# Kernel optimization log

Measured on AMD Instinct MI355X. Metric: run time of the kernel, lower is better.

Reference implementation:

```python
import jax, jax.numpy as jnp
import numpy as np

BETA = 0.9
THRESHOLD = 1.0
N_IN, N_HID, N_OUT = 784, 2048, 10
BATCH = 128
T_STEPS = 32


def _spike(x):
    # snnTorch heaviside fire: spk = 1 where (mem - threshold) > 0
    return (x > 0).astype(x.dtype)


def setup_inputs() -> dict:
    key = jax.random.key(0)
    ks = jax.random.split(key, 6)

    def lin(k, fan_in, fan_out):
        bound = 1.0 / np.sqrt(fan_in)
        kw, kb = jax.random.split(k)
        W = jax.random.uniform(kw, (fan_out, fan_in), minval=-bound, maxval=bound, dtype=jnp.float32)
        b = jax.random.uniform(kb, (fan_out,), minval=-bound, maxval=bound, dtype=jnp.float32)
        return W, b

    W0, b0 = lin(ks[0], N_IN, N_HID)
    W1, b1 = lin(ks[1], N_HID, N_HID)
    W2, b2 = lin(ks[2], N_HID, N_HID)
    W3, b3 = lin(ks[3], N_HID, N_HID)
    W4, b4 = lin(ks[4], N_HID, N_OUT)
    input_tensor = jax.random.uniform(ks[5], (BATCH, N_IN), dtype=jnp.float32)
    return {"input_tensor": input_tensor,
            "W0": W0, "W1": W1, "W2": W2, "W3": W3, "W4": W4,
            "b0": b0, "b1": b1, "b2": b2, "b3": b3, "b4": b4,
            "time_steps": T_STEPS}


def reference(input_tensor, W0, W1, W2, W3, W4, b0, b1, b2, b3, b4, time_steps):
    Ws = [W0, W1, W2, W3, W4]
    bs = [b0, b1, b2, b3, b4]
    n_lif = len(Ws) + 1  # 6 LIF layers
    batch = input_tensor.shape[0]
    dims = [N_IN, N_HID, N_HID, N_HID, N_HID, N_OUT]  # membrane shapes per LIF
    dtype = input_tensor.dtype

    def step(mems, _):
        cur = input_tensor  # same static input injected every step (as in the torch loop)
        new_mems = []
        var_list = []
        count_list = []
        spk_last = None
        for i in range(n_lif):
            # snnTorch Leaky (reset_mechanism='subtract'):
            # reset computed from PREVIOUS membrane (detached), then decay + input
            reset = jax.lax.stop_gradient((mems[i] > THRESHOLD).astype(dtype))
            mem = BETA * mems[i] + cur - reset * THRESHOLD
            spk = _spike(mem - THRESHOLD)
            new_mems.append(mem)
            count_list.append(spk.sum(axis=1).mean(axis=0))  # sum over features, mean over batch
            if i < n_lif - 1:
                var_list.append(jnp.var(mem, ddof=1))  # torch.var default: unbiased
                cur = spk @ Ws[i].T + bs[i]
            else:
                spk_last = spk
        return tuple(new_mems), (spk_last, jnp.stack(var_list), jnp.stack(count_list))

    mems0 = tuple(jnp.zeros((batch, d), dtype=dtype) for d in dims)
    _, (spike_out, vars_t, counts_t) = jax.lax.scan(step, mems0, None, length=time_steps)

    mean_var_mems = vars_t.mean(axis=0)                       # [n_linears] = [5]
    normalized_spike_counts = counts_t.sum(axis=0) / (time_steps * batch)  # [n_lif] = [6]
    return mean_var_mems, spike_out, normalized_spike_counts
```

## Files before the change

kernel.cpp:

```cpp
#include <hip/hip_runtime.h>
#include <stdint.h>

#define BETA 0.9f
#define NIN 784
#define KA0 832
#define NHID 2048
#define BATCH 128
#define TSTEPS 32
#define MROWS 4096

typedef float f32x4 __attribute__((ext_vector_type(4)));
typedef int   i32x4 __attribute__((ext_vector_type(4)));

#define S1F 0x1p-11f
#define S2F 0x1p-19f
#define S3F 0x1p-27f

__device__ __forceinline__ float nofuse(float x) {
  asm volatile("" : "+v"(x));
  return x;
}

typedef __attribute__((address_space(1))) const unsigned int gas_uint;
typedef __attribute__((address_space(3))) unsigned int las_uint;
__device__ __forceinline__ void gload_lds16(const void* g, void* l) {
  __builtin_amdgcn_global_load_lds((gas_uint*)g, (las_uint*)l, 16, 0, 0);
}

static const size_t SZ_WS0  = (size_t)3 * 2048 * KA0;
static const size_t SZ_WSH  = (size_t)3 * 2048 * 2048;
static const size_t SZ_W4T  = (size_t)2048 * 16 * 4;
static const size_t SZ_SPK  = (size_t)MROWS * 2048;
static const size_t SZ_CUR  = (size_t)MROWS * 2048 * 4;
static const size_t SZ_CUR5 = (size_t)MROWS * 16 * 4;
static const size_t SZ_VST  = (size_t)5 * TSTEPS * 256 * 2 * 4;
static const size_t SZ_CST  = (size_t)6 * TSTEPS * 256 * 4;

static const size_t OFF_WS0  = 0;
static const size_t OFF_WS1  = OFF_WS0 + SZ_WS0;
static const size_t OFF_WS2  = OFF_WS1 + SZ_WSH;
static const size_t OFF_WS3  = OFF_WS2 + SZ_WSH;
static const size_t OFF_W4T  = OFF_WS3 + SZ_WSH;
static const size_t OFF_SPKA = OFF_W4T + SZ_W4T;
static const size_t OFF_SPKB = OFF_SPKA + SZ_SPK;
static const size_t OFF_CUR  = OFF_SPKB + SZ_SPK;
static const size_t OFF_CUR5 = OFF_CUR + SZ_CUR;
static const size_t OFF_VST  = OFF_CUR5 + SZ_CUR5;
static const size_t OFF_CST  = OFF_VST + SZ_VST;

__global__ void k_wsplit(const float* __restrict__ W, signed char* __restrict__ dst,
                         int nrows, int kvalid, int kpad) {
  int idx = blockIdx.x * blockDim.x + threadIdx.x;
  int kq = kvalid >> 2;
  if (idx >= nrows * kq) return;
  int row = idx / kq, k0 = (idx - row * kq) * 4;
  const float* src = W + (size_t)row * kvalid + k0;
  signed char p1[4], p2[4], p3[4];
#pragma unroll
  for (int e = 0; e < 4; ++e) {
    float f = src[e];
    float q1 = rintf(f * 2048.0f);
    float r1 = f - q1 * S1F;
    float q2 = rintf(r1 * 524288.0f);
    q2 = fminf(127.f, fmaxf(-127.f, q2));
    float r2 = r1 - q2 * S2F;
    float q3 = rintf(r2 * 134217728.0f);
    q3 = fminf(127.f, fmaxf(-127.f, q3));
    p1[e] = (signed char)(int)q1;
    p2[e] = (signed char)(int)q2;
    p3[e] = (signed char)(int)q3;
  }
  size_t base = (size_t)row * kpad + k0;
  size_t plane = (size_t)nrows * kpad;
  *(char4*)(dst + base)             = make_char4(p1[0], p1[1], p1[2], p1[3]);
  *(char4*)(dst + plane + base)     = make_char4(p2[0], p2[1], p2[2], p2[3]);
  *(char4*)(dst + 2 * plane + base) = make_char4(p3[0], p3[1], p3[2], p3[3]);
}

__global__ void k_w4t(const float* __restrict__ W4, float* __restrict__ w4t) {
  int k = blockIdx.x * blockDim.x + threadIdx.x;
  if (k >= 2048) return;
#pragma unroll
  for (int c = 0; c < 16; ++c)
    w4t[(size_t)k * 16 + c] = (c < 10) ? W4[(size_t)c * 2048 + k] : 0.f;
}

__global__ __launch_bounds__(256, 2) void k_gemm3p(
    const signed char* __restrict__ A,
    const signed char* __restrict__ B,
    float* __restrict__ C,
    int N, int Ka) {
  __shared__ __align__(16) signed char smem[2][32768];
  const int tid = threadIdx.x;
  const int lane = tid & 63, wv = tid >> 6;

  const int bid = blockIdx.x;
  const int xcd = bid & 7, lid = bid >> 3;
  const int by = (xcd >> 1) * 8 + (lid >> 3);
  const int bx = (xcd & 1) * 8 + (lid & 7);
  const int m0 = by * 128, n0 = bx * 128;
  const int NT = Ka >> 6;

  i32x4 acc0[4][4], acc1[4][4], acc2[4][4];
#pragma unroll
  for (int i = 0; i < 4; ++i)
#pragma unroll
    for (int j = 0; j < 4; ++j) {
      acc0[i][j] = (i32x4){0, 0, 0, 0};
      acc1[i][j] = (i32x4){0, 0, 0, 0};
      acc2[i][j] = (i32x4){0, 0, 0, 0};
    }

  auto stage_part = [&](int buf, int kt, int i0, int i1) {
    const int koff = kt * 64;
    const signed char* Abase = A + (size_t)m0 * Ka + koff;
    for (int i = i0; i < i1; ++i) {
      int c = i * 256 + tid;
      const signed char* src;
      if (c < 512) {
        int row = c >> 2, kb = c & 3;
        int gkb = kb ^ ((row >> 1) & 3);
        src = Abase + (size_t)row * Ka + gkb * 16;
      } else {
        int cb = c - 512;
        int s = cb >> 9, cc = cb & 511;
        int row = cc >> 2, kb = cc & 3;
        int gkb = kb ^ ((row >> 1) & 3);
        src = B + ((size_t)s * N + n0 + row) * Ka + koff + gkb * 16;
      }
      gload_lds16(src, &smem[buf][(i * 256 + wv * 64) * 16]);
    }
  };

  const int wm = wv >> 1, wn = wv & 1;
  const int g = lane >> 4, rr = lane & 15;

  auto readA = [&](int p, i32x4* a) {
#pragma unroll
    for (int mf = 0; mf < 4; ++mf) {
      int row = wm * 64 + mf * 16 + rr;
      int slot = g ^ ((row >> 1) & 3);
      a[mf] = *(const i32x4*)&smem[p][row * 64 + slot * 16];
    }
  };
  auto readB = [&](int p, int s, i32x4* b) {
#pragma unroll
    for (int nf = 0; nf < 4; ++nf) {
      int row = wn * 64 + nf * 16 + rr;
      int slot = g ^ ((row >> 1) & 3);
      b[nf] = *(const i32x4*)&smem[p][8192 + s * 8192 + row * 64 + slot * 16];
    }
  };
  auto cluster = [&](i32x4* a, i32x4* b, i32x4 (*acc)[4]) {
    __builtin_amdgcn_s_setprio(1);
#pragma unroll
    for (int mf = 0; mf < 4; ++mf)
#pragma unroll
      for (int nf = 0; nf < 4; ++nf)
        acc[mf][nf] = __builtin_amdgcn_mfma_i32_16x16x64_i8(a[mf], b[nf], acc[mf][nf], 0, 0, 0);
    __builtin_amdgcn_s_setprio(0);
  };

#define PHASE_SYNC(nimm)                                   \
  asm volatile("s_waitcnt vmcnt(" #nimm ")" ::: "memory"); \
  __builtin_amdgcn_sched_barrier(0);                       \
  __builtin_amdgcn_s_barrier();                            \
  __builtin_amdgcn_sched_barrier(0);

  stage_part(0, 0, 0, 8);

  for (int kt = 0; kt < NT - 1; ++kt) {
    const int p = kt & 1;
    i32x4 a[4], b[4];
    PHASE_SYNC(4)
    stage_part(p ^ 1, kt + 1, 0, 2);
    readA(p, a);
    readB(p, 0, b);
    cluster(a, b, acc0);
    PHASE_SYNC(4)
    stage_part(p ^ 1, kt + 1, 2, 6);
    readB(p, 1, b);
    cluster(a, b, acc1);
    PHASE_SYNC(6)
    stage_part(p ^ 1, kt + 1, 6, 8);
    readB(p, 2, b);
    cluster(a, b, acc2);
  }
  {
    const int p = (NT - 1) & 1;
    i32x4 a[4], b[4];
    PHASE_SYNC(4)
    readA(p, a);
    readB(p, 0, b);
    cluster(a, b, acc0);
    PHASE_SYNC(2)
    readB(p, 1, b);
    cluster(a, b, acc1);
    PHASE_SYNC(0)
    readB(p, 2, b);
    cluster(a, b, acc2);
  }
#undef PHASE_SYNC

#pragma unroll
  for (int mf = 0; mf < 4; ++mf)
#pragma unroll
    for (int nf = 0; nf < 4; ++nf) {
      int col = n0 + wn * 64 + nf * 16 + rr;
#pragma unroll
      for (int v = 0; v < 4; ++v) {
        int row = m0 + wm * 64 + mf * 16 + g * 4 + v;
        float f = S1F * (float)acc0[mf][nf][v];
        f = __fmaf_rn(S2F, (float)acc1[mf][nf][v], f);
        f = __fmaf_rn(S3F, (float)acc2[mf][nf][v], f);
        C[(size_t)row * N + col] = f;
      }
    }
}

__global__ __launch_bounds__(128) void k_scan0(
    const float* __restrict__ input, signed char* __restrict__ spk0,
    float* __restrict__ vstats, int* __restrict__ cstats) {
  const int b = blockIdx.x, tid = threadIdx.x;
  const int j0 = tid * 8;
  const bool act = (j0 < NIN);
  const int lane = tid & 63, wv = tid >> 6;
  __shared__ float ssum[2][TSTEPS], ssq[2][TSTEPS];
  __shared__ int scnt[2][TSTEPS];
  float iv[8];
  if (act) {
    const float* ip = input + (size_t)b * NIN + j0;
    float4 c0 = *(const float4*)ip, c1 = *(const float4*)(ip + 4);
    iv[0]=c0.x; iv[1]=c0.y; iv[2]=c0.z; iv[3]=c0.w;
    iv[4]=c1.x; iv[5]=c1.y; iv[6]=c1.z; iv[7]=c1.w;
  } else {
#pragma unroll
    for (int e = 0; e < 8; ++e) iv[e] = 0.f;
  }
  float mem[8] = {0,0,0,0,0,0,0,0};
  for (int t = 0; t < TSTEPS; ++t) {
    float sum = 0.f, sq = 0.f; int cnt = 0;
    unsigned long long pk = 0;
#pragma unroll
    for (int e = 0; e < 8; ++e) {
      float reset = mem[e] > 1.0f ? 1.0f : 0.0f;
      float t1 = nofuse(BETA * mem[e]);
      float t2 = nofuse(t1 + iv[e]);
      float mn = t2 - reset;
      mem[e] = mn;
      int s = mn > 1.0f;
      pk |= (unsigned long long)(s ? 1u : 0u) << (8 * e);
      sum += mn; sq = __fmaf_rn(mn, mn, sq); cnt += s;
    }
    if (act)
      *(unsigned long long*)(spk0 + (size_t)(t * BATCH + b) * KA0 + j0) = pk;
#pragma unroll
    for (int o = 32; o > 0; o >>= 1) {
      sum += __shfl_down(sum, o, 64);
      sq  += __shfl_down(sq, o, 64);
      cnt += __shfl_down(cnt, o, 64);
    }
    if (lane == 0) { ssum[wv][t] = sum; ssq[wv][t] = sq; scnt[wv][t] = cnt; }
  }
  __syncthreads();
  if (tid < TSTEPS) {
    int t = tid;
    float s = ssum[0][t] + ssum[1][t];
    float q = ssq[0][t] + ssq[1][t];
    int c = scnt[0][t] + scnt[1][t];
    vstats[((size_t)(0 * TSTEPS + t) * 256 + b) * 2 + 0] = s;
    vstats[((size_t)(0 * TSTEPS + t) * 256 + b) * 2 + 1] = q;
    cstats[(0 * TSTEPS + t) * 256 + b] = c;
  }
}

__global__ __launch_bounds__(128) void k_scan(
    const float* __restrict__ cur, const float* __restrict__ bias,
    signed char* __restrict__ spk, float* __restrict__ vstats,
    int* __restrict__ cstats, int layer) {
  const int blk = blockIdx.x;
  const int b = blk >> 1, half = blk & 1;
  const int tid = threadIdx.x;
  const int j0 = half * 1024 + tid * 8;
  const int lane = tid & 63, wv = tid >> 6;
  __shared__ float ssum[2][TSTEPS], ssq[2][TSTEPS];
  __shared__ int scnt[2][TSTEPS];
  float bs[8];
  {
    const float* bp = bias + j0;
    float4 c0 = *(const float4*)bp, c1 = *(const float4*)(bp + 4);
    bs[0]=c0.x; bs[1]=c0.y; bs[2]=c0.z; bs[3]=c0.w;
    bs[4]=c1.x; bs[5]=c1.y; bs[6]=c1.z; bs[7]=c1.w;
  }
  float mem[8] = {0,0,0,0,0,0,0,0};
  for (int t = 0; t < TSTEPS; ++t) {
    size_t off = (size_t)(t * BATCH + b) * 2048 + j0;
    const float* cp = cur + off;
    float4 c0 = *(const float4*)cp, c1 = *(const float4*)(cp + 4);
    float cv[8] = {c0.x, c0.y, c0.z, c0.w, c1.x, c1.y, c1.z, c1.w};
    float sum = 0.f, sq = 0.f; int cnt = 0;
    unsigned long long pk = 0;
#pragma unroll
    for (int e = 0; e < 8; ++e) {
      float cc = nofuse(cv[e] + bs[e]);
      float reset = mem[e] > 1.0f ? 1.0f : 0.0f;
      float t1 = nofuse(BETA * mem[e]);
      float t2 = nofuse(t1 + cc);
      float mn = t2 - reset;
      mem[e] = mn;
      int s = mn > 1.0f;
      pk |= (unsigned long long)(s ? 1u : 0u) << (8 * e);
      sum += mn; sq = __fmaf_rn(mn, mn, sq); cnt += s;
    }
    *(unsigned long long*)(spk + (size_t)(t * BATCH + b) * 2048 + j0) = pk;
#pragma unroll
    for (int o = 32; o > 0; o >>= 1) {
      sum += __shfl_down(sum, o, 64);
      sq  += __shfl_down(sq, o, 64);
      cnt += __shfl_down(cnt, o, 64);
    }
    if (lane == 0) { ssum[wv][t] = sum; ssq[wv][t] = sq; scnt[wv][t] = cnt; }
  }
  __syncthreads();
  if (tid < TSTEPS) {
    int t = tid;
    float s = ssum[0][t] + ssum[1][t];
    float q = ssq[0][t] + ssq[1][t];
    int c = scnt[0][t] + scnt[1][t];
    vstats[((size_t)(layer * TSTEPS + t) * 256 + blk) * 2 + 0] = s;
    vstats[((size_t)(layer * TSTEPS + t) * 256 + blk) * 2 + 1] = q;
    cstats[(layer * TSTEPS + t) * 256 + blk] = c;
  }
}

__global__ __launch_bounds__(256) void k_gemm4(
    const signed char* __restrict__ spk, const float* __restrict__ w4t,
    float* __restrict__ out) {
  int idx = blockIdx.x * 256 + threadIdx.x;
  int r = idx >> 4, c = idx & 15;
  const signed char* sp = spk + (size_t)r * 2048;
  float acc = 0.f;
  for (int k = 0; k < 2048; k += 4) {
    char4 s4 = *(const char4*)(sp + k);
    acc = __fmaf_rn((float)s4.x, w4t[(size_t)(k + 0) * 16 + c], acc);
    acc = __fmaf_rn((float)s4.y, w4t[(size_t)(k + 1) * 16 + c], acc);
    acc = __fmaf_rn((float)s4.z, w4t[(size_t)(k + 2) * 16 + c], acc);
    acc = __fmaf_rn((float)s4.w, w4t[(size_t)(k + 3) * 16 + c], acc);
  }
  out[(size_t)r * 16 + c] = acc;
}

__global__ __launch_bounds__(640) void k_scan5(
    const float* __restrict__ cur5, const float* __restrict__ b4,
    float* __restrict__ spike_out, int* __restrict__ cstats) {
  const int tid = threadIdx.x;
  const int idx = blockIdx.x * 640 + tid;
  const int b = idx / 10, j = idx - b * 10;
  const int lane = tid & 63, wv = tid >> 6;
  __shared__ int scnt[10][TSTEPS];
  const float bias = b4[j];
  float mem = 0.f;
  for (int t = 0; t < TSTEPS; ++t) {
    float cc = nofuse(cur5[(size_t)(t * BATCH + b) * 16 + j] + bias);
    float reset = mem > 1.0f ? 1.0f : 0.0f;
    float t1 = nofuse(BETA * mem);
    float t2 = nofuse(t1 + cc);
    float mn = t2 - reset;
    mem = mn;
    int s = mn > 1.0f;
    spike_out[(size_t)t * 1280 + b * 10 + j] = s ? 1.0f : 0.0f;
    int cnt = s;
#pragma unroll
    for (int o = 32; o > 0; o >>= 1) cnt += __shfl_down(cnt, o, 64);
    if (lane == 0) scnt[wv][t] = cnt;
  }
  __syncthreads();
  if (tid < TSTEPS) {
    int t = tid, c = 0;
#pragma unroll
    for (int w = 0; w < 10; ++w) c += scnt[w][t];
    cstats[(5 * TSTEPS + t) * 256 + blockIdx.x] = c;
  }
}

__global__ __launch_bounds__(512) void k_final(
    const float* __restrict__ vstats, const int* __restrict__ cstats,
    float* __restrict__ d_out) {
  __shared__ float varLDS[5][TSTEPS];
  __shared__ float cntLDS[6][TSTEPS];
  int tid = threadIdx.x;
  if (tid < 160) {
    int l = tid / 32, t = tid - l * 32;
    double s = 0.0, q = 0.0;
    for (int b = 0; b < 256; ++b) {
      s += (double)vstats[((size_t)(l * TSTEPS + t) * 256 + b) * 2 + 0];
      q += (double)vstats[((size_t)(l * TSTEPS + t) * 256 + b) * 2 + 1];
    }
    double n = (l == 0) ? (double)(BATCH * NIN) : (double)(BATCH * NHID);
    varLDS[l][t] = (float)((q - s * s / n) / (n - 1.0));
  } else if (tid < 352) {
    int i = (tid - 160) / 32, t = (tid - 160) - i * 32;
    int c = 0;
    for (int b = 0; b < 256; ++b) c += cstats[(i * TSTEPS + t) * 256 + b];
    cntLDS[i][t] = (float)c * (1.0f / 128.0f);
  }
  __syncthreads();
  if (tid < 5) {
    float a = 0.f;
    for (int t = 0; t < TSTEPS; ++t) a = __fadd_rn(a, varLDS[tid][t]);
    d_out[tid] = a / 32.0f;
  } else if (tid >= 8 && tid < 14) {
    int i = tid - 8;
    float a = 0.f;
    for (int t = 0; t < TSTEPS; ++t) a = __fadd_rn(a, cntLDS[i][t]);
    d_out[40965 + i] = a / 4096.0f;
  }
}

extern "C" void kernel_launch(void* const* d_in, const int* in_sizes, int n_in,
                              void* d_out, int out_size, void* d_ws, size_t ws_size,
                              hipStream_t stream) {
  const float* input = (const float*)d_in[0];
  const float* W0 = (const float*)d_in[1];
  const float* W1 = (const float*)d_in[2];
  const float* W2 = (const float*)d_in[3];
  const float* W3 = (const float*)d_in[4];
  const float* W4 = (const float*)d_in[5];
  const float* b0 = (const float*)d_in[6];
  const float* b1 = (const float*)d_in[7];
  const float* b2 = (const float*)d_in[8];
  const float* b3 = (const float*)d_in[9];
  const float* b4 = (const float*)d_in[10];

  uint8_t* ws = (uint8_t*)d_ws;
  signed char* ws0  = (signed char*)(ws + OFF_WS0);
  signed char* ws1  = (signed char*)(ws + OFF_WS1);
  signed char* ws2  = (signed char*)(ws + OFF_WS2);
  signed char* ws3  = (signed char*)(ws + OFF_WS3);
  float* w4t        = (float*)(ws + OFF_W4T);
  signed char* spkA = (signed char*)(ws + OFF_SPKA);
  signed char* spkB = (signed char*)(ws + OFF_SPKB);
  float* cur        = (float*)(ws + OFF_CUR);
  float* cur5       = (float*)(ws + OFF_CUR5);
  float* vst        = (float*)(ws + OFF_VST);
  int* cst          = (int*)(ws + OFF_CST);
  float* out        = (float*)d_out;

  hipMemsetAsync(ws + OFF_VST, 0, SZ_VST + SZ_CST, stream);
  hipMemsetAsync(ws + OFF_SPKA, 0, (size_t)TSTEPS * BATCH * KA0, stream);
  hipMemsetAsync(ws + OFF_WS0, 0, SZ_WS0, stream);

  {
    int thr = 2048 * (NIN / 4);
    k_wsplit<<<(thr + 255) / 256, 256, 0, stream>>>(W0, ws0, 2048, NIN, KA0);
  }
  {
    int thr = 2048 * (2048 / 4);
    int gb = (thr + 255) / 256;
    k_wsplit<<<gb, 256, 0, stream>>>(W1, ws1, 2048, 2048, 2048);
    k_wsplit<<<gb, 256, 0, stream>>>(W2, ws2, 2048, 2048, 2048);
    k_wsplit<<<gb, 256, 0, stream>>>(W3, ws3, 2048, 2048, 2048);
  }
  k_w4t<<<8, 256, 0, stream>>>(W4, w4t);

  k_scan0<<<BATCH, 128, 0, stream>>>(input, spkA, vst, cst);
  k_gemm3p<<<512, 256, 0, stream>>>(spkA, ws0, cur, 2048, KA0);
  k_scan<<<256, 128, 0, stream>>>(cur, b0, spkB, vst, cst, 1);
  k_gemm3p<<<512, 256, 0, stream>>>(spkB, ws1, cur, 2048, 2048);
  k_scan<<<256, 128, 0, stream>>>(cur, b1, spkA, vst, cst, 2);
  k_gemm3p<<<512, 256, 0, stream>>>(spkA, ws2, cur, 2048, 2048);
  k_scan<<<256, 128, 0, stream>>>(cur, b2, spkB, vst, cst, 3);
  k_gemm3p<<<512, 256, 0, stream>>>(spkB, ws3, cur, 2048, 2048);
  k_scan<<<256, 128, 0, stream>>>(cur, b3, spkA, vst, cst, 4);
  k_gemm4<<<256, 256, 0, stream>>>(spkA, w4t, cur5);
  k_scan5<<<2, 640, 0, stream>>>(cur5, b4, out + 5, cst);
  k_final<<<1, 512, 0, stream>>>(vst, cst, out);
}
```

Before: 402.0 us.

## Merge weight-split launches, simplify GEMM staging to one sync per k-tile, widen final reduction

Combines the four weight quantization-split kernels into a single launch to cut launch overhead. Replaces the GEMM's three-phase partial staging and waitcnt scheme with one full-tile prefetch per iteration behind a single barrier, folding the epilogue iteration into the loop. Doubles the threads in the final statistics reduction and combines thread pairs with a shuffle. The simpler GEMM pipeline may give up some of the load/MFMA interleaving the phased version had.

```diff
diff --git a/kernel.cpp b/kernel.cpp
--- a/kernel.cpp
+++ b/kernel.cpp
@@ -48,9 +48,9 @@
 static const size_t OFF_VST  = OFF_CUR5 + SZ_CUR5;
 static const size_t OFF_CST  = OFF_VST + SZ_VST;
 
-__global__ void k_wsplit(const float* __restrict__ W, signed char* __restrict__ dst,
-                         int nrows, int kvalid, int kpad) {
-  int idx = blockIdx.x * blockDim.x + threadIdx.x;
+__device__ __forceinline__ void wsplit_one(const float* __restrict__ W,
+                                           signed char* __restrict__ dst,
+                                           int idx, int nrows, int kvalid, int kpad) {
   int kq = kvalid >> 2;
   if (idx >= nrows * kq) return;
   int row = idx / kq, k0 = (idx - row * kq) * 4;
@@ -77,6 +77,23 @@
   *(char4*)(dst + 2 * plane + base) = make_char4(p3[0], p3[1], p3[2], p3[3]);
 }
 
+__global__ void k_wsplit_all(const float* __restrict__ W0, const float* __restrict__ W1,
+                             const float* __restrict__ W2, const float* __restrict__ W3,
+                             signed char* __restrict__ d0, signed char* __restrict__ d1,
+                             signed char* __restrict__ d2, signed char* __restrict__ d3) {
+  int blk = blockIdx.x;
+  if (blk < 1568) {
+    wsplit_one(W0, d0, blk * 256 + threadIdx.x, 2048, NIN, KA0);
+  } else {
+    int j = blk - 1568;
+    int w = j >> 12, r = j & 4095;
+    int idx = r * 256 + threadIdx.x;
+    if (w == 0)      wsplit_one(W1, d1, idx, 2048, 2048, 2048);
+    else if (w == 1) wsplit_one(W2, d2, idx, 2048, 2048, 2048);
+    else             wsplit_one(W3, d3, idx, 2048, 2048, 2048);
+  }
+}
+
 __global__ void k_w4t(const float* __restrict__ W4, float* __restrict__ w4t) {
   int k = blockIdx.x * blockDim.x + threadIdx.x;
   if (k >= 2048) return;
@@ -111,10 +128,11 @@
       acc2[i][j] = (i32x4){0, 0, 0, 0};
     }
 
-  auto stage_part = [&](int buf, int kt, int i0, int i1) {
+  auto stage_all = [&](int buf, int kt) {
     const int koff = kt * 64;
     const signed char* Abase = A + (size_t)m0 * Ka + koff;
-    for (int i = i0; i < i1; ++i) {
+#pragma unroll
+    for (int i = 0; i < 8; ++i) {
       int c = i * 256 + tid;
       const signed char* src;
       if (c < 512) {
@@ -161,46 +179,26 @@
     __builtin_amdgcn_s_setprio(0);
   };
 
-#define PHASE_SYNC(nimm)                                   \
-  asm volatile("s_waitcnt vmcnt(" #nimm ")" ::: "memory"); \
-  __builtin_amdgcn_sched_barrier(0);                       \
-  __builtin_amdgcn_s_barrier();                            \
-  __builtin_amdgcn_sched_barrier(0);
-
-  stage_part(0, 0, 0, 8);
-
-  for (int kt = 0; kt < NT - 1; ++kt) {
+  stage_all(0, 0);
+
+  for (int kt = 0; kt < NT; ++kt) {
     const int p = kt & 1;
+    asm volatile("s_waitcnt vmcnt(0)" ::: "memory");
+    __builtin_amdgcn_sched_barrier(0);
+    __builtin_amdgcn_s_barrier();
+    __builtin_amdgcn_sched_barrier(0);
+
+    if (kt + 1 < NT) stage_all(p ^ 1, kt + 1);
+
     i32x4 a[4], b[4];
-    PHASE_SYNC(4)
-    stage_part(p ^ 1, kt + 1, 0, 2);
     readA(p, a);
     readB(p, 0, b);
     cluster(a, b, acc0);
-    PHASE_SYNC(4)
-    stage_part(p ^ 1, kt + 1, 2, 6);
     readB(p, 1, b);
     cluster(a, b, acc1);
-    PHASE_SYNC(6)
-    stage_part(p ^ 1, kt + 1, 6, 8);
     readB(p, 2, b);
     cluster(a, b, acc2);
   }
-  {
-    const int p = (NT - 1) & 1;
-    i32x4 a[4], b[4];
-    PHASE_SYNC(4)
-    readA(p, a);
-    readB(p, 0, b);
-    cluster(a, b, acc0);
-    PHASE_SYNC(2)
-    readB(p, 1, b);
-    cluster(a, b, acc1);
-    PHASE_SYNC(0)
-    readB(p, 2, b);
-    cluster(a, b, acc2);
-  }
-#undef PHASE_SYNC
 
 #pragma unroll
   for (int mf = 0; mf < 4; ++mf)
@@ -383,26 +381,34 @@
   }
 }
 
-__global__ __launch_bounds__(512) void k_final(
+__global__ __launch_bounds__(1024) void k_final(
     const float* __restrict__ vstats, const int* __restrict__ cstats,
     float* __restrict__ d_out) {
   __shared__ float varLDS[5][TSTEPS];
   __shared__ float cntLDS[6][TSTEPS];
   int tid = threadIdx.x;
-  if (tid < 160) {
-    int l = tid / 32, t = tid - l * 32;
+  if (tid < 320) {
+    int j = tid >> 1, par = tid & 1;
+    int l = j >> 5, t = j & 31;
     double s = 0.0, q = 0.0;
-    for (int b = 0; b < 256; ++b) {
-      s += (double)vstats[((size_t)(l * TSTEPS + t) * 256 + b) * 2 + 0];
-      q += (double)vstats[((size_t)(l * TSTEPS + t) * 256 + b) * 2 + 1];
-    }
-    double n = (l == 0) ? (double)(BATCH * NIN) : (double)(BATCH * NHID);
-    varLDS[l][t] = (float)((q - s * s / n) / (n - 1.0));
-  } else if (tid < 352) {
-    int i = (tid - 160) / 32, t = (tid - 160) - i * 32;
+    for (int b = par; b < 256; b += 2) {
+      s += (double)vstats[((size_t)j * 256 + b) * 2 + 0];
+      q += (double)vstats[((size_t)j * 256 + b) * 2 + 1];
+    }
+    s += __shfl_xor(s, 1, 64);
+    q += __shfl_xor(q, 1, 64);
+    if (par == 0) {
+      double n = (l == 0) ? (double)(BATCH * NIN) : (double)(BATCH * NHID);
+      varLDS[l][t] = (float)((q - s * s / n) / (n - 1.0));
+    }
+  } else if (tid >= 384 && tid < 768) {
+    int jj = tid - 384;
+    int j = jj >> 1, par = jj & 1;
+    int i = j >> 5, t = j & 31;
     int c = 0;
-    for (int b = 0; b < 256; ++b) c += cstats[(i * TSTEPS + t) * 256 + b];
-    cntLDS[i][t] = (float)c * (1.0f / 128.0f);
+    for (int b = par; b < 256; b += 2) c += cstats[j * 256 + b];
+    c += __shfl_xor(c, 1, 64);
+    if (par == 0) cntLDS[i][t] = (float)c * (1.0f / 128.0f);
   }
   __syncthreads();
   if (tid < 5) {
@@ -450,17 +456,7 @@
   hipMemsetAsync(ws + OFF_SPKA, 0, (size_t)TSTEPS * BATCH * KA0, stream);
   hipMemsetAsync(ws + OFF_WS0, 0, SZ_WS0, stream);
 
-  {
-    int thr = 2048 * (NIN / 4);
-    k_wsplit<<<(thr + 255) / 256, 256, 0, stream>>>(W0, ws0, 2048, NIN, KA0);
-  }
-  {
-    int thr = 2048 * (2048 / 4);
-    int gb = (thr + 255) / 256;
-    k_wsplit<<<gb, 256, 0, stream>>>(W1, ws1, 2048, 2048, 2048);
-    k_wsplit<<<gb, 256, 0, stream>>>(W2, ws2, 2048, 2048, 2048);
-    k_wsplit<<<gb, 256, 0, stream>>>(W3, ws3, 2048, 2048, 2048);
-  }
+  k_wsplit_all<<<1568 + 3 * 4096, 256, 0, stream>>>(W0, W1, W2, W3, ws0, ws1, ws2, ws3);
   k_w4t<<<8, 256, 0, stream>>>(W4, w4t);
 
   k_scan0<<<BATCH, 128, 0, stream>>>(input, spkA, vst, cst);
@@ -474,5 +470,5 @@
   k_scan<<<256, 128, 0, stream>>>(cur, b3, spkA, vst, cst, 4);
   k_gemm4<<<256, 256, 0, stream>>>(spkA, w4t, cur5);
   k_scan5<<<2, 640, 0, stream>>>(cur5, b4, out + 5, cst);
-  k_final<<<1, 512, 0, stream>>>(vst, cst, out);
-}
+  k_final<<<1, 1024, 0, stream>>>(vst, cst, out);
+}
```

New measurement: 410.0 us. Within noise of the previous version (+2.0%).
